# Kernel optimization log

Measured on AMD Instinct MI355X. Metric: run time of the kernel, lower is better.

Reference implementation:

```python
import jax, jax.numpy as jnp
import numpy as np

N_NODES = 50000
N_EDGES = 800000
IN_CH = 128
HID = 256
N_GRAPHS = 512


def setup_inputs() -> dict:
    key = jax.random.key(0)
    ks = jax.random.split(key, 10)
    x = jax.random.normal(ks[0], (N_NODES, IN_CH), dtype=jnp.float32)
    edge_index = jax.random.randint(ks[1], (2, N_EDGES), 0, N_NODES, dtype=jnp.int32)
    batch = jnp.sort(jax.random.randint(ks[2], (N_NODES,), 0, N_GRAPHS, dtype=jnp.int32))
    # GCNConv params (glorot-ish init)
    W0 = jax.random.normal(ks[3], (IN_CH, HID), dtype=jnp.float32) / np.sqrt(IN_CH)
    b0 = jnp.zeros((HID,), dtype=jnp.float32)
    W1 = jax.random.normal(ks[4], (HID, HID), dtype=jnp.float32) / np.sqrt(HID)
    b1 = jnp.zeros((HID,), dtype=jnp.float32)
    W2 = jax.random.normal(ks[5], (HID, HID), dtype=jnp.float32) / np.sqrt(HID)
    b2 = jnp.zeros((HID,), dtype=jnp.float32)
    return {"x": x, "W0": W0, "b0": b0, "W1": W1, "b1": b1, "W2": W2, "b2": b2,
            "edge_index": edge_index, "batch": batch}


def _gcn_norm(edge_index, num_nodes):
    # PyG gcn_norm with add_self_loops=True: A_hat = A + I, norm = D^-1/2 A_hat D^-1/2
    src, dst = edge_index[0], edge_index[1]
    loop = jnp.arange(num_nodes, dtype=src.dtype)
    src = jnp.concatenate([src, loop])
    dst = jnp.concatenate([dst, loop])
    deg = jax.ops.segment_sum(jnp.ones_like(dst, dtype=jnp.float32), dst,
                              num_segments=num_nodes)
    dinv = jnp.where(deg > 0, jax.lax.rsqrt(deg), 0.0)
    norm = dinv[src] * dinv[dst]  # [E + N]
    return src, dst, norm


def _gcn_conv(x, W, b, src, dst, norm, num_nodes):
    h = x @ W                                  # [N, out]
    msg = norm[:, None] * h[src]               # gather + scale, [E+N, out]
    out = jax.ops.segment_sum(msg, dst, num_segments=num_nodes)  # scatter-add
    return out + b


def reference(x, W0, b0, W1, b1, W2, b2, edge_index, batch):
    n = x.shape[0]
    src, dst, norm = _gcn_norm(edge_index, n)  # normalization is layer-independent
    h = jax.nn.relu(_gcn_conv(x, W0, b0, src, dst, norm, n))
    h = jax.nn.relu(_gcn_conv(h, W1, b1, src, dst, norm, n))
    h = jax.nn.relu(_gcn_conv(h, W2, b2, src, dst, norm, n))
    # global_add_pool: segment-sum node features by graph id
    return jax.ops.segment_sum(h, batch, num_segments=N_GRAPHS)
```

## Files before the change

### kernel.cpp

```cpp
#include <hip/hip_runtime.h>
#include <hip/hip_fp16.h>

constexpr int NN  = 50000;
constexpr int NE  = 800000;
constexpr int CIN = 128;
constexpr int CH  = 256;
constexpr int NG  = 512;

typedef unsigned short ushort_t;
typedef unsigned int uint_t;

static __device__ __forceinline__ ushort_t f2bf(float f) {
    uint_t u = __float_as_uint(f);
    u += 0x7fffu + ((u >> 16) & 1u);
    return (ushort_t)(u >> 16);
}

static __device__ __forceinline__ float h16tof(uint_t bits) {
    return __half2float(__ushort_as_half((unsigned short)bits));
}

__global__ void conv_x_kernel(const float4* __restrict__ x, ushort4* __restrict__ xb, int n4) {
    int i = blockIdx.x * blockDim.x + threadIdx.x;
    if (i >= n4) return;
    float4 v = x[i];
    ushort4 o;
    o.x = f2bf(v.x); o.y = f2bf(v.y); o.z = f2bf(v.z); o.w = f2bf(v.w);
    xb[i] = o;
}

__global__ void conv_wt_kernel(const float* __restrict__ W, ushort_t* __restrict__ Wt, int K, int N) {
    int i = blockIdx.x * blockDim.x + threadIdx.x;
    if (i >= K * N) return;
    int k = i / N, n = i % N;
    Wt[(size_t)n * K + k] = f2bf(W[i]);
}

__global__ void count_kernel(const int* __restrict__ dst, int* __restrict__ cnt, int E) {
    int e = blockIdx.x * blockDim.x + threadIdx.x;
    if (e < E) atomicAdd(&cnt[dst[e]], 1);
}

__global__ __launch_bounds__(256) void scan_bsum_kernel(const int* __restrict__ cnt,
                                                        int* __restrict__ bsum, int n) {
    int i = blockIdx.x * 256 + threadIdx.x;
    int v = (i < n) ? ((cnt[i] + 7) & ~7) : 0;
    #pragma unroll
    for (int off = 32; off >= 1; off >>= 1) v += __shfl_xor(v, off, 64);
    __shared__ int ws[4];
    if ((threadIdx.x & 63) == 0) ws[threadIdx.x >> 6] = v;
    __syncthreads();
    if (threadIdx.x == 0) bsum[blockIdx.x] = ws[0] + ws[1] + ws[2] + ws[3];
}

__global__ __launch_bounds__(256) void scan_boff_kernel(int* __restrict__ bsum, int nb) {
    int tid = threadIdx.x, lane = tid & 63, wid = tid >> 6;
    int v = (tid < nb) ? bsum[tid] : 0;
    int s = v;
    #pragma unroll
    for (int off = 1; off < 64; off <<= 1) {
        int t = __shfl_up(s, off, 64);
        if (lane >= off) s += t;
    }
    __shared__ int wsum[4];
    if (lane == 63) wsum[wid] = s;
    __syncthreads();
    int wadd = 0;
    #pragma unroll
    for (int w = 0; w < 4; w++) if (w < wid) wadd += wsum[w];
    if (tid < nb) bsum[tid] = wadd + s - v;
}

__global__ __launch_bounds__(256) void scan_final_kernel(const int* __restrict__ cnt,
                                                         const int* __restrict__ boff,
                                                         int* __restrict__ rowptr,
                                                         float* __restrict__ dinv, int n) {
    int tid = threadIdx.x, lane = tid & 63, wid = tid >> 6;
    int i = blockIdx.x * 256 + tid;
    int c = (i < n) ? cnt[i] : 0;
    int v = (c + 7) & ~7;
    int s = v;
    #pragma unroll
    for (int off = 1; off < 64; off <<= 1) {
        int t = __shfl_up(s, off, 64);
        if (lane >= off) s += t;
    }
    __shared__ int wsum[4];
    if (lane == 63) wsum[wid] = s;
    __syncthreads();
    int wadd = boff[blockIdx.x];
    #pragma unroll
    for (int w = 0; w < 4; w++) if (w < wid) wadd += wsum[w];
    if (i < n) {
        rowptr[i] = wadd + s - v;
        dinv[i]   = rsqrtf((float)c + 1.0f);
        if (i == n - 1) rowptr[n] = wadd + s;
    }
}

__global__ void scatter_kernel(const int* __restrict__ src, const int* __restrict__ dst,
                               const int* __restrict__ rowptr, int* __restrict__ cursor,
                               const float* __restrict__ dinv, uint_t* __restrict__ epack, int E) {
    int e = blockIdx.x * blockDim.x + threadIdx.x;
    if (e >= E) return;
    int d = dst[e];
    int s = src[e];
    int p = rowptr[d] + atomicAdd(&cursor[d], 1);
    uint_t hb = (uint_t)__half_as_ushort(__float2half(dinv[s]));
    epack[p] = (uint_t)s | (hb << 16);
}

template <int C, int MODE>
__global__ __launch_bounds__(256) void node_agg_kernel(
    const ushort_t* __restrict__ h, const int* __restrict__ rowptr,
    const int* __restrict__ degc, const uint_t* __restrict__ epack,
    const float* __restrict__ dinv, const float* __restrict__ bias,
    const int* __restrict__ batch, void* __restrict__ out_v, int n) {
    constexpr int V = C / 64;
    int wave = threadIdx.x >> 6;
    int lane = threadIdx.x & 63;
    int d = blockIdx.x * 4 + wave;
    if (d >= n) return;

    int beg = __builtin_amdgcn_readfirstlane(rowptr[d]);
    int deg = __builtin_amdgcn_readfirstlane(degc[d]);
    const uint_t* hu = (const uint_t*)h;

    float acc[V] = {};
    const uint4* ep4 = (const uint4*)(epack + beg);
    uint4 ea, eb, na, nb;
    if (deg > 0) { ea = ep4[0]; eb = ep4[1]; }

    for (int e = 0; e < deg; e += 8) {
        int blk = e >> 3;
        if (e + 8 < deg) { na = ep4[blk * 2 + 2]; nb = ep4[blk * 2 + 3]; }
        uint_t eps[8] = {ea.x, ea.y, ea.z, ea.w, eb.x, eb.y, eb.z, eb.w};
        int   srcs[8];
        float wts[8];
        #pragma unroll
        for (int u = 0; u < 8; u++) {
            bool a = (e + u) < deg;
            srcs[u] = a ? (int)(eps[u] & 0xffffu) : d;
            wts[u]  = a ? h16tof(eps[u] >> 16) : 0.0f;
        }
        if constexpr (V == 4) {
            uint_t ra[8], rb[8];
            #pragma unroll
            for (int u = 0; u < 8; u++) {
                const uint_t* row = hu + (size_t)__builtin_amdgcn_readfirstlane(srcs[u]) * (C / 2);
                ra[u] = row[lane];
                rb[u] = row[64 + lane];
            }
            #pragma unroll
            for (int u = 0; u < 8; u++) {
                float w = wts[u];
                acc[0] += w * __uint_as_float(ra[u] << 16);
                acc[1] += w * __uint_as_float(ra[u] & 0xffff0000u);
                acc[2] += w * __uint_as_float(rb[u] << 16);
                acc[3] += w * __uint_as_float(rb[u] & 0xffff0000u);
            }
        } else {
            uint_t rv[8];
            #pragma unroll
            for (int u = 0; u < 8; u++) {
                const uint_t* row = hu + (size_t)__builtin_amdgcn_readfirstlane(srcs[u]) * (C / 2);
                rv[u] = row[lane];
            }
            #pragma unroll
            for (int u = 0; u < 8; u++) {
                float w = wts[u];
                acc[0] += w * __uint_as_float(rv[u] << 16);
                acc[1] += w * __uint_as_float(rv[u] & 0xffff0000u);
            }
        }
        ea = na; eb = nb;
    }

    float dd = dinv[d];
    float self[V];
    {
        const uint_t* row = hu + (size_t)d * (C / 2);
        uint_t sa = row[lane];
        self[0] = __uint_as_float(sa << 16);
        self[1] = __uint_as_float(sa & 0xffff0000u);
        if constexpr (V == 4) {
            uint_t sb = row[64 + lane];
            self[2] = __uint_as_float(sb << 16);
            self[3] = __uint_as_float(sb & 0xffff0000u);
        }
    }

    float r[V];
    if constexpr (MODE >= 1) {
        float2 bA = *(const float2*)(bias + 2 * lane);
        r[0] = fmaxf(dd * acc[0] + dd * dd * self[0] + bA.x, 0.0f);
        r[1] = fmaxf(dd * acc[1] + dd * dd * self[1] + bA.y, 0.0f);
        if constexpr (V == 4) {
            float2 bB = *(const float2*)(bias + 128 + 2 * lane);
            r[2] = fmaxf(dd * acc[2] + dd * dd * self[2] + bB.x, 0.0f);
            r[3] = fmaxf(dd * acc[3] + dd * dd * self[3] + bB.y, 0.0f);
        }
    } else {
        #pragma unroll
        for (int i = 0; i < V; i++)
            r[i] = dd * acc[i] + dd * dd * self[i];
    }

    if constexpr (MODE == 2) {
        float* o = (float*)out_v + (size_t)batch[d] * C;
        atomicAdd(o + 2 * lane, r[0]);
        atomicAdd(o + 2 * lane + 1, r[1]);
        if constexpr (V == 4) {
            atomicAdd(o + 128 + 2 * lane, r[2]);
            atomicAdd(o + 128 + 2 * lane + 1, r[3]);
        }
    } else {
        uint_t* o = (uint_t*)((ushort_t*)out_v + (size_t)d * C);
        o[lane] = (uint_t)f2bf(r[0]) | ((uint_t)f2bf(r[1]) << 16);
        if constexpr (V == 4)
            o[64 + lane] = (uint_t)f2bf(r[2]) | ((uint_t)f2bf(r[3]) << 16);
    }
}

typedef __attribute__((ext_vector_type(8))) short bf16x8;
typedef __attribute__((ext_vector_type(4))) float f32x4;

template <int MODE>
__global__ __launch_bounds__(256) void gemm_bf16_kernel(
    const ushort_t* __restrict__ A, const ushort_t* __restrict__ Wt,
    const float* __restrict__ bias, ushort_t* __restrict__ C, int M, int K) {
    __shared__ ushort_t As[128][40];
    __shared__ ushort_t Bs[128][40];
    int tid = threadIdx.x;
    int row0 = blockIdx.x * 128, col0 = blockIdx.y * 128;
    int lr = tid >> 2, lq = tid & 3;
    int lane = tid & 63, wv = tid >> 6;
    int wr = (wv >> 1) * 64, wc = (wv & 1) * 64;
    int r16 = lane & 15, quad = lane >> 4;

    f32x4 acc[4][4] = {};

    for (int k0 = 0; k0 < K; k0 += 32) {
        {
            int gr0 = row0 + lr, gr1 = row0 + lr + 64;
            uint4 a0 = make_uint4(0, 0, 0, 0), a1 = make_uint4(0, 0, 0, 0);
            if (gr0 < M) a0 = *(const uint4*)(A + (size_t)gr0 * K + k0 + lq * 8);
            if (gr1 < M) a1 = *(const uint4*)(A + (size_t)gr1 * K + k0 + lq * 8);
            *(uint4*)&As[lr][lq * 8]      = a0;
            *(uint4*)&As[lr + 64][lq * 8] = a1;
            uint4 b0 = *(const uint4*)(Wt + (size_t)(col0 + lr) * K + k0 + lq * 8);
            uint4 b1 = *(const uint4*)(Wt + (size_t)(col0 + lr + 64) * K + k0 + lq * 8);
            *(uint4*)&Bs[lr][lq * 8]      = b0;
            *(uint4*)&Bs[lr + 64][lq * 8] = b1;
        }
        __syncthreads();
        bf16x8 af[4], bfr[4];
        #pragma unroll
        for (int i = 0; i < 4; i++) af[i]  = *(const bf16x8*)&As[wr + i * 16 + r16][quad * 8];
        #pragma unroll
        for (int j = 0; j < 4; j++) bfr[j] = *(const bf16x8*)&Bs[wc + j * 16 + r16][quad * 8];
        #pragma unroll
        for (int i = 0; i < 4; i++)
            #pragma unroll
            for (int j = 0; j < 4; j++)
                acc[i][j] = __builtin_amdgcn_mfma_f32_16x16x32_bf16(af[i], bfr[j], acc[i][j], 0, 0, 0);
        __syncthreads();
    }

    #pragma unroll
    for (int j = 0; j < 4; j++) {
        int colc = col0 + wc + j * 16 + r16;
        float bval = (MODE == 1) ? bias[colc] : 0.0f;
        #pragma unroll
        for (int i = 0; i < 4; i++) {
            #pragma unroll
            for (int r = 0; r < 4; r++) {
                int row = row0 + wr + i * 16 + quad * 4 + r;
                if (row < M) {
                    float v = acc[i][j][r];
                    if (MODE == 1) v = fmaxf(v + bval, 0.0f);
                    C[(size_t)row * 256 + colc] = f2bf(v);
                }
            }
        }
    }
}

extern "C" void kernel_launch(void* const* d_in, const int* in_sizes, int n_in,
                              void* d_out, int out_size, void* d_ws, size_t ws_size,
                              hipStream_t stream) {
    const float* x   = (const float*)d_in[0];
    const float* W0  = (const float*)d_in[1];
    const float* b0  = (const float*)d_in[2];
    const float* W1  = (const float*)d_in[3];
    const float* b1  = (const float*)d_in[4];
    const float* W2  = (const float*)d_in[5];
    const float* b2  = (const float*)d_in[6];
    const int*   ei  = (const int*)d_in[7];
    const int*   src = ei;
    const int*   dst = ei + NE;
    const int*   batch = (const int*)d_in[8];
    float* out = (float*)d_out;

    char* ws = (char*)d_ws;
    ushort_t* Abf = (ushort_t*)ws;
    ushort_t* Bbf = (ushort_t*)(ws + 25600000ull);
    ushort_t* xbf = (ushort_t*)(ws + 51200000ull);
    ushort_t* W0t = (ushort_t*)(ws + 64000000ull);
    ushort_t* W1t = (ushort_t*)(ws + 64065536ull);
    ushort_t* W2t = (ushort_t*)(ws + 64196608ull);
    float*    dinv   = (float*)(ws + 64327680ull);
    int*      rowptr = (int*)  (ws + 64527680ull);
    int*      cnt    = (int*)  (ws + 64727808ull);
    uint_t*   epack  = (uint_t*)(ws + 64927808ull);
    int*      bsum   = (int*)  (ws + 71327808ull);
    int*      cursor = (int*)ws;

    const int scanBlocks = (NN + 255) / 256;
    const int nodeBlocks = (NN + 3) / 4;
    const dim3 ggrid((NN + 127) / 128, 2);

    conv_x_kernel<<<(NN * CIN / 4 + 255) / 256, 256, 0, stream>>>((const float4*)x, (ushort4*)xbf, NN * CIN / 4);
    conv_wt_kernel<<<(CIN * CH + 255) / 256, 256, 0, stream>>>(W0, W0t, CIN, CH);
    conv_wt_kernel<<<(CH * CH + 255) / 256, 256, 0, stream>>>(W1, W1t, CH, CH);
    conv_wt_kernel<<<(CH * CH + 255) / 256, 256, 0, stream>>>(W2, W2t, CH, CH);

    hipMemsetAsync(cnt, 0, (size_t)NN * 4, stream);
    count_kernel<<<(NE + 255) / 256, 256, 0, stream>>>(dst, cnt, NE);
    scan_bsum_kernel<<<scanBlocks, 256, 0, stream>>>(cnt, bsum, NN);
    scan_boff_kernel<<<1, 256, 0, stream>>>(bsum, scanBlocks);
    scan_final_kernel<<<scanBlocks, 256, 0, stream>>>(cnt, bsum, rowptr, dinv, NN);
    hipMemsetAsync(cursor, 0, (size_t)NN * 4, stream);
    scatter_kernel<<<(NE + 255) / 256, 256, 0, stream>>>(src, dst, rowptr, cursor, dinv, epack, NE);

    node_agg_kernel<CIN, 0><<<nodeBlocks, 256, 0, stream>>>(xbf, rowptr, cnt, epack, dinv, nullptr, nullptr, Bbf, NN);
    gemm_bf16_kernel<1><<<ggrid, 256, 0, stream>>>(Bbf, W0t, b0, Abf, NN, CIN);

    gemm_bf16_kernel<0><<<ggrid, 256, 0, stream>>>(Abf, W1t, nullptr, Bbf, NN, CH);
    node_agg_kernel<CH, 1><<<nodeBlocks, 256, 0, stream>>>(Bbf, rowptr, cnt, epack, dinv, b1, nullptr, Abf, NN);

    gemm_bf16_kernel<0><<<ggrid, 256, 0, stream>>>(Abf, W2t, nullptr, Bbf, NN, CH);
    hipMemsetAsync(out, 0, (size_t)NG * CH * 4, stream);
    node_agg_kernel<CH, 2><<<nodeBlocks, 256, 0, stream>>>(Bbf, rowptr, cnt, epack, dinv, b2, batch, out, NN);
}
```

Measured before the change: 442.1 us.

## Store layer-1/2 GEMM outputs in FP8 and gather FP8 in aggregation

The GEMMs for layers 1 and 2 now write their outputs as FP8 bytes instead of bf16, and a new node aggregation kernel gathers and decodes these FP8 rows. Each lane handles four channels, which halves the bytes moved by the gather-heavy neighbour reads. The change also merges the three weight-conversion kernels into one launch and uses nontemporal stores for the aggregation outputs. FP8 intermediates lose a lot of precision and may break the accuracy tolerance.

After: 489.3 us. 1.11x slower.

```diff
diff --git a/kernel.cpp b/kernel.cpp
--- a/kernel.cpp
+++ b/kernel.cpp
@@ -9,6 +9,9 @@
 
 typedef unsigned short ushort_t;
 typedef unsigned int uint_t;
+typedef unsigned char uchar_t;
+typedef __attribute__((ext_vector_type(2))) float f32x2_t;
+typedef __attribute__((ext_vector_type(2))) uint_t u32x2_t;
 
 static __device__ __forceinline__ ushort_t f2bf(float f) {
     uint_t u = __float_as_uint(f);
@@ -29,11 +32,22 @@
     xb[i] = o;
 }
 
-__global__ void conv_wt_kernel(const float* __restrict__ W, ushort_t* __restrict__ Wt, int K, int N) {
+__global__ void conv_wt3_kernel(const float* __restrict__ W0, const float* __restrict__ W1,
+                                const float* __restrict__ W2, ushort_t* __restrict__ W0t,
+                                ushort_t* __restrict__ W1t, ushort_t* __restrict__ W2t) {
     int i = blockIdx.x * blockDim.x + threadIdx.x;
-    if (i >= K * N) return;
-    int k = i / N, n = i % N;
-    Wt[(size_t)n * K + k] = f2bf(W[i]);
+    if (i < 32768) {
+        int k = i >> 8, n = i & 255;
+        W0t[n * 128 + k] = f2bf(W0[i]);
+    } else if (i < 98304) {
+        int j = i - 32768;
+        int k = j >> 8, n = j & 255;
+        W1t[n * 256 + k] = f2bf(W1[j]);
+    } else if (i < 163840) {
+        int j = i - 98304;
+        int k = j >> 8, n = j & 255;
+        W2t[n * 256 + k] = f2bf(W2[j]);
+    }
 }
 
 __global__ void count_kernel(const int* __restrict__ dst, int* __restrict__ cnt, int E) {
@@ -216,19 +230,95 @@
         }
     } else {
         uint_t* o = (uint_t*)((ushort_t*)out_v + (size_t)d * C);
-        o[lane] = (uint_t)f2bf(r[0]) | ((uint_t)f2bf(r[1]) << 16);
+        __builtin_nontemporal_store((uint_t)f2bf(r[0]) | ((uint_t)f2bf(r[1]) << 16), &o[lane]);
         if constexpr (V == 4)
-            o[64 + lane] = (uint_t)f2bf(r[2]) | ((uint_t)f2bf(r[3]) << 16);
+            __builtin_nontemporal_store((uint_t)f2bf(r[2]) | ((uint_t)f2bf(r[3]) << 16), &o[64 + lane]);
+    }
+}
+
+template <int MODE>
+__global__ __launch_bounds__(256) void node_agg_fp8_kernel(
+    const uchar_t* __restrict__ h8, const int* __restrict__ rowptr,
+    const int* __restrict__ degc, const uint_t* __restrict__ epack,
+    const float* __restrict__ dinv, const float* __restrict__ bias,
+    const int* __restrict__ batch, void* __restrict__ out_v, int n) {
+    int wave = threadIdx.x >> 6;
+    int lane = threadIdx.x & 63;
+    int d = blockIdx.x * 4 + wave;
+    if (d >= n) return;
+
+    int beg = __builtin_amdgcn_readfirstlane(rowptr[d]);
+    int deg = __builtin_amdgcn_readfirstlane(degc[d]);
+    const uint_t* hu = (const uint_t*)h8;
+
+    float a0 = 0.0f, a1 = 0.0f, a2 = 0.0f, a3 = 0.0f;
+    const uint4* ep4 = (const uint4*)(epack + beg);
+    uint4 ea, eb, na, nb;
+    if (deg > 0) { ea = ep4[0]; eb = ep4[1]; }
+
+    for (int e = 0; e < deg; e += 8) {
+        int blk = e >> 3;
+        if (e + 8 < deg) { na = ep4[blk * 2 + 2]; nb = ep4[blk * 2 + 3]; }
+        uint_t eps[8] = {ea.x, ea.y, ea.z, ea.w, eb.x, eb.y, eb.z, eb.w};
+        int   srcs[8];
+        float wts[8];
+        #pragma unroll
+        for (int u = 0; u < 8; u++) {
+            bool a = (e + u) < deg;
+            srcs[u] = a ? (int)(eps[u] & 0xffffu) : d;
+            wts[u]  = a ? h16tof(eps[u] >> 16) : 0.0f;
+        }
+        uint_t rv[8];
+        #pragma unroll
+        for (int u = 0; u < 8; u++)
+            rv[u] = hu[(size_t)__builtin_amdgcn_readfirstlane(srcs[u]) * 64 + lane];
+        #pragma unroll
+        for (int u = 0; u < 8; u++) {
+            float w = wts[u];
+            f32x2_t lo = __builtin_amdgcn_cvt_pk_f32_fp8(rv[u], false);
+            f32x2_t hi = __builtin_amdgcn_cvt_pk_f32_fp8(rv[u], true);
+            a0 += w * lo.x;
+            a1 += w * lo.y;
+            a2 += w * hi.x;
+            a3 += w * hi.y;
+        }
+        ea = na; eb = nb;
+    }
+
+    float dd = dinv[d];
+    uint_t sv = hu[(size_t)d * 64 + lane];
+    f32x2_t slo = __builtin_amdgcn_cvt_pk_f32_fp8(sv, false);
+    f32x2_t shi = __builtin_amdgcn_cvt_pk_f32_fp8(sv, true);
+
+    float4 b4 = *(const float4*)(bias + 4 * lane);
+    float dd2 = dd * dd;
+    float r0 = fmaxf(dd * a0 + dd2 * slo.x + b4.x, 0.0f);
+    float r1 = fmaxf(dd * a1 + dd2 * slo.y + b4.y, 0.0f);
+    float r2 = fmaxf(dd * a2 + dd2 * shi.x + b4.z, 0.0f);
+    float r3 = fmaxf(dd * a3 + dd2 * shi.y + b4.w, 0.0f);
+
+    if constexpr (MODE == 2) {
+        float* o = (float*)out_v + (size_t)batch[d] * CH + 4 * lane;
+        atomicAdd(o + 0, r0);
+        atomicAdd(o + 1, r1);
+        atomicAdd(o + 2, r2);
+        atomicAdd(o + 3, r3);
+    } else {
+        u32x2_t st;
+        st.x = (uint_t)f2bf(r0) | ((uint_t)f2bf(r1) << 16);
+        st.y = (uint_t)f2bf(r2) | ((uint_t)f2bf(r3) << 16);
+        u32x2_t* o = (u32x2_t*)((ushort_t*)out_v + (size_t)d * CH) + lane;
+        __builtin_nontemporal_store(st, o);
     }
 }
 
 typedef __attribute__((ext_vector_type(8))) short bf16x8;
 typedef __attribute__((ext_vector_type(4))) float f32x4;
 
-template <int MODE>
+template <int MODE, int F8OUT>
 __global__ __launch_bounds__(256) void gemm_bf16_kernel(
     const ushort_t* __restrict__ A, const ushort_t* __restrict__ Wt,
-    const float* __restrict__ bias, ushort_t* __restrict__ C, int M, int K) {
+    const float* __restrict__ bias, void* __restrict__ Cv, int M, int K) {
     __shared__ ushort_t As[128][40];
     __shared__ ushort_t Bs[128][40];
     int tid = threadIdx.x;
@@ -279,7 +369,12 @@
                 if (row < M) {
                     float v = acc[i][j][r];
                     if (MODE == 1) v = fmaxf(v + bval, 0.0f);
-                    C[(size_t)row * 256 + colc] = f2bf(v);
+                    if constexpr (F8OUT) {
+                        uint_t pk = __builtin_amdgcn_cvt_pk_fp8_f32(v, v, 0u, false);
+                        ((uchar_t*)Cv)[(size_t)row * 256 + colc] = (uchar_t)(pk & 0xffu);
+                    } else {
+                        ((ushort_t*)Cv)[(size_t)row * 256 + colc] = f2bf(v);
+                    }
                 }
             }
         }
@@ -303,8 +398,9 @@
     float* out = (float*)d_out;
 
     char* ws = (char*)d_ws;
-    ushort_t* Abf = (ushort_t*)ws;
-    ushort_t* Bbf = (ushort_t*)(ws + 25600000ull);
+    ushort_t* P1  = (ushort_t*)ws;
+    ushort_t* G0  = (ushort_t*)(ws + 25600000ull);
+    uchar_t*  F8  = (uchar_t*) (ws + 38400000ull);
     ushort_t* xbf = (ushort_t*)(ws + 51200000ull);
     ushort_t* W0t = (ushort_t*)(ws + 64000000ull);
     ushort_t* W1t = (ushort_t*)(ws + 64065536ull);
@@ -321,9 +417,7 @@
     const dim3 ggrid((NN + 127) / 128, 2);
 
     conv_x_kernel<<<(NN * CIN / 4 + 255) / 256, 256, 0, stream>>>((const float4*)x, (ushort4*)xbf, NN * CIN / 4);
-    conv_wt_kernel<<<(CIN * CH + 255) / 256, 256, 0, stream>>>(W0, W0t, CIN, CH);
-    conv_wt_kernel<<<(CH * CH + 255) / 256, 256, 0, stream>>>(W1, W1t, CH, CH);
-    conv_wt_kernel<<<(CH * CH + 255) / 256, 256, 0, stream>>>(W2, W2t, CH, CH);
+    conv_wt3_kernel<<<640, 256, 0, stream>>>(W0, W1, W2, W0t, W1t, W2t);
 
     hipMemsetAsync(cnt, 0, (size_t)NN * 4, stream);
     count_kernel<<<(NE + 255) / 256, 256, 0, stream>>>(dst, cnt, NE);
@@ -333,13 +427,13 @@
     hipMemsetAsync(cursor, 0, (size_t)NN * 4, stream);
     scatter_kernel<<<(NE + 255) / 256, 256, 0, stream>>>(src, dst, rowptr, cursor, dinv, epack, NE);
 
-    node_agg_kernel<CIN, 0><<<nodeBlocks, 256, 0, stream>>>(xbf, rowptr, cnt, epack, dinv, nullptr, nullptr, Bbf, NN);
-    gemm_bf16_kernel<1><<<ggrid, 256, 0, stream>>>(Bbf, W0t, b0, Abf, NN, CIN);
-
-    gemm_bf16_kernel<0><<<ggrid, 256, 0, stream>>>(Abf, W1t, nullptr, Bbf, NN, CH);
-    node_agg_kernel<CH, 1><<<nodeBlocks, 256, 0, stream>>>(Bbf, rowptr, cnt, epack, dinv, b1, nullptr, Abf, NN);
-
-    gemm_bf16_kernel<0><<<ggrid, 256, 0, stream>>>(Abf, W2t, nullptr, Bbf, NN, CH);
+    node_agg_kernel<CIN, 0><<<nodeBlocks, 256, 0, stream>>>(xbf, rowptr, cnt, epack, dinv, nullptr, nullptr, G0, NN);
+    gemm_bf16_kernel<1, 0><<<ggrid, 256, 0, stream>>>(G0, W0t, b0, P1, NN, CIN);
+
+    gemm_bf16_kernel<0, 1><<<ggrid, 256, 0, stream>>>(P1, W1t, nullptr, F8, NN, CH);
+    node_agg_fp8_kernel<1><<<nodeBlocks, 256, 0, stream>>>(F8, rowptr, cnt, epack, dinv, b1, nullptr, P1, NN);
+
+    gemm_bf16_kernel<0, 1><<<ggrid, 256, 0, stream>>>(P1, W2t, nullptr, F8, NN, CH);
     hipMemsetAsync(out, 0, (size_t)NG * CH * 4, stream);
-    node_agg_kernel<CH, 2><<<nodeBlocks, 256, 0, stream>>>(Bbf, rowptr, cnt, epack, dinv, b2, batch, out, NN);
-}
+    node_agg_fp8_kernel<2><<<nodeBlocks, 256, 0, stream>>>(F8, rowptr, cnt, epack, dinv, b2, batch, out, NN);
+}
```
